# Kernel optimization log

Hardware: AMD Instinct MI355X
Metric: run time of the kernel (lower is better)

## Reference

```python
import jax, jax.numpy as jnp
import numpy as np

NUM_LAYERS = 3

def setup_inputs() -> dict:
    key = jax.random.key(0)
    k1, k2, k3, k4 = jax.random.split(key, 4)
    N, D, E = 100000, 128, 3200000
    x = jax.random.normal(k1, (N, D), dtype=jnp.float32)
    edge_row = jax.random.randint(k2, (E,), 0, N, dtype=jnp.int64 if jax.config.jax_enable_x64 else jnp.int32)
    edge_col = jax.random.randint(k3, (E,), 0, N, dtype=jnp.int64 if jax.config.jax_enable_x64 else jnp.int32)
    # normalized-adjacency-like positive values
    edge_val = jax.random.uniform(k4, (E,), dtype=jnp.float32)
    return {"x": x, "edge_row": edge_row, "edge_col": edge_col, "edge_val": edge_val}

def _spmm(edge_row, edge_col, edge_val, emb, num_nodes):
    # out[r] += val * emb[c]  -- sparse adjacency @ emb
    msgs = edge_val[:, None] * emb[edge_col]          # [E, D] gather + scale
    return jax.ops.segment_sum(msgs, edge_row, num_segments=num_nodes)

def reference(x, edge_row, edge_col, edge_val):
    N = x.shape[0]
    emb = x
    acc = x  # running sum over layer embeddings (layer 0 included)
    for _ in range(NUM_LAYERS):
        emb = _spmm(edge_row, edge_col, edge_val, emb, N)
        acc = acc + emb
    # mean over (num_layers + 1) stacked embeddings, without materializing the stack
    return acc / jnp.float32(NUM_LAYERS + 1)
```

## Files before the change

### kernel.cpp

```cpp
#include <hip/hip_runtime.h>

#define DIMS 128
#define RPB 64
#define CAP 3072
#define NBK_MAX 1600
#define NBINS 1024

typedef _Float16 half_t;
typedef _Float16 half2_t __attribute__((ext_vector_type(2)));

static __device__ __forceinline__ unsigned halfbits(float v) {
    half_t h = (half_t)v;
    unsigned short us;
    __builtin_memcpy(&us, &h, 2);
    return (unsigned)us;
}
static __device__ __forceinline__ half2_t h2(int b) { return __builtin_bit_cast(half2_t, b); }
static __device__ __forceinline__ int ih(half2_t h) { return __builtin_bit_cast(int, h); }

__global__ void cvt_kernel(const float* __restrict__ src, half_t* __restrict__ dst, int n2) {
    int i = blockIdx.x * blockDim.x + threadIdx.x;
    if (i >= n2) return;
    float2 v = reinterpret_cast<const float2*>(src)[i];
    half2_t h;
    h.x = (half_t)v.x;
    h.y = (half_t)v.y;
    reinterpret_cast<half2_t*>(&dst[0])[i] = h;
}

__global__ __launch_bounds__(512) void binA_kernel(
    const int* __restrict__ row, const int* __restrict__ col,
    const float* __restrict__ val, int E, int nbk,
    int* __restrict__ fill, int2* __restrict__ staged) {
    __shared__ int cnt[NBK_MAX];
    __shared__ int base[NBK_MAX];
    const int t = threadIdx.x;
    const int tile0 = blockIdx.x * 8192;
    for (int j = t; j < nbk; j += 512) cnt[j] = 0;
    __syncthreads();
    for (int k = 0; k < 4; ++k) {
        int e = tile0 + (k * 512 + t) * 4;
        if (e + 3 < E) {
            int4 r4 = *reinterpret_cast<const int4*>(&row[e]);
            atomicAdd(&cnt[r4.x >> 6], 1);
            atomicAdd(&cnt[r4.y >> 6], 1);
            atomicAdd(&cnt[r4.z >> 6], 1);
            atomicAdd(&cnt[r4.w >> 6], 1);
        } else {
            for (int j = e; j < E; ++j) atomicAdd(&cnt[row[j] >> 6], 1);
        }
    }
    __syncthreads();
    for (int j = t; j < nbk; j += 512) {
        int c = cnt[j];
        base[j] = c ? atomicAdd(&fill[j], c) : 0;
        cnt[j] = 0;
    }
    __syncthreads();
    for (int k = 0; k < 4; ++k) {
        int e = tile0 + (k * 512 + t) * 4;
        int n = (e + 3 < E) ? 4 : max(0, E - e);
        if (n == 4) {
            int4 r4 = *reinterpret_cast<const int4*>(&row[e]);
            int4 c4 = *reinterpret_cast<const int4*>(&col[e]);
            float4 v4 = *reinterpret_cast<const float4*>(&val[e]);
            int rr[4] = {r4.x, r4.y, r4.z, r4.w};
            int cc[4] = {c4.x, c4.y, c4.z, c4.w};
            float vv[4] = {v4.x, v4.y, v4.z, v4.w};
#pragma unroll
            for (int j = 0; j < 4; ++j) {
                int b = rr[j] >> 6;
                int p = base[b] + atomicAdd(&cnt[b], 1);
                if (p < CAP) {
                    unsigned hb = halfbits(vv[j]);
                    int2 pk;
                    pk.x = (int)(((unsigned)(rr[j] & 63) << 26) | ((unsigned)cc[j] << 8));
                    pk.y = (int)((hb << 16) | hb);
                    staged[(size_t)b * CAP + p] = pk;
                }
            }
        } else {
            for (int j = e; j < e + n; ++j) {
                int r = row[j];
                int b = r >> 6;
                int p = base[b] + atomicAdd(&cnt[b], 1);
                if (p < CAP) {
                    unsigned hb = halfbits(val[j]);
                    int2 pk;
                    pk.x = (int)(((unsigned)(r & 63) << 26) | ((unsigned)col[j] << 8));
                    pk.y = (int)((hb << 16) | hb);
                    staged[(size_t)b * CAP + p] = pk;
                }
            }
        }
    }
}

__global__ __launch_bounds__(512) void sort_bucket(
    const int* __restrict__ fill, int2* __restrict__ staged,
    int* __restrict__ rowinfo, int N) {
    __shared__ int2 outb[CAP];
    __shared__ int cur[NBINS];
    __shared__ int wsum[8];
    const int b = blockIdx.x;
    const int t = threadIdx.x;
    const int w = t >> 6, lane = t & 63;
    const int cnt = min(fill[b], CAP);
    int2* gb = staged + (size_t)b * CAP;

    cur[2 * t] = 0;
    cur[2 * t + 1] = 0;
    __syncthreads();
    for (int i = t; i < cnt; i += 512) {
        unsigned k = (unsigned)gb[i].x;
        int key = (int)((k >> 26) << 4) | (int)((k >> 21) & 0xF);
        atomicAdd(&cur[key], 1);
    }
    __syncthreads();
    int h0 = cur[2 * t], h1 = cur[2 * t + 1];
    int s = h0 + h1;
    int v = s;
    for (int d = 1; d < 64; d <<= 1) {
        int u = __shfl_up(v, d, 64);
        if (lane >= d) v += u;
    }
    if (lane == 63) wsum[w] = v;
    __syncthreads();
    if (t < 8) {
        int ws = wsum[t];
        int vv = ws;
        for (int d = 1; d < 8; d <<= 1) {
            int u = __shfl_up(vv, d, 64);
            if (t >= d) vv += u;
        }
        wsum[t] = vv - ws;
    }
    __syncthreads();
    int excl = wsum[w] + (v - s);
    cur[2 * t] = excl;
    cur[2 * t + 1] = excl + h0;
    __syncthreads();
    if (t < RPB) {
        int start = cur[t * 16];
        int end = (t == RPB - 1) ? cnt : cur[t * 16 + 16];
        int r = b * RPB + t;
        if (r < N) rowinfo[r] = (start << 16) | end;
    }
    __syncthreads();
    for (int i = t; i < cnt; i += 512) {
        int2 pk = gb[i];
        unsigned k = (unsigned)pk.x;
        int key = (int)((k >> 26) << 4) | (int)((k >> 21) & 0xF);
        int p = atomicAdd(&cur[key], 1);
        outb[p] = pk;
    }
    __syncthreads();
    for (int i = t; i < cnt; i += 512) gb[i] = outb[i];
}

template <int MODE>
__global__ __launch_bounds__(256) void spmm_kernel(
    const half_t* __restrict__ emb_in, const int* __restrict__ rowinfo,
    const int2* __restrict__ staged, int N,
    half_t* __restrict__ emb_out, half_t* __restrict__ acc_h,
    float* __restrict__ out) {
    const int r = (blockIdx.x * blockDim.x + threadIdx.x) >> 6;
    const int lane = threadIdx.x & 63;
    if (r >= N) return;
    const int info = rowinfo[r];
    const int start = info >> 16;
    const int end = info & 0xFFFF;
    const int2* eb = staged + (size_t)(r >> 6) * CAP;
    const char* tbl = reinterpret_cast<const char*>(emb_in);
    const int g = lane >> 4;
    const unsigned q16 = (unsigned)(lane & 15) << 4;

    half2_t acc[4][4];
#pragma unroll
    for (int u = 0; u < 4; ++u)
#pragma unroll
        for (int s = 0; s < 4; ++s) acc[u][s] = (half2_t)0;

    for (int base = start; base < end; base += 64) {
        const int cnt = min(64, end - base);
        int2 myE = make_int2(0, 0);
        if (base + lane < end) myE = eb[base + lane];

        int k = 0;
        for (; k + 16 <= cnt; k += 16) {
            int ex[4], ey[4];
#pragma unroll
            for (int u = 0; u < 4; ++u) {
                ex[u] = __shfl(myE.x, k + 4 * u + g, 64);
                ey[u] = __shfl(myE.y, k + 4 * u + g, 64);
            }
            int4 tv[4];
#pragma unroll
            for (int u = 0; u < 4; ++u) {
                unsigned voff = ((unsigned)ex[u] & 0x03FFFF00u) + q16;
                tv[u] = *reinterpret_cast<const int4*>(tbl + voff);
            }
#pragma unroll
            for (int u = 0; u < 4; ++u) {
                half2_t vv = h2(ey[u]);
                acc[u][0] = h2(tv[u].x) * vv + acc[u][0];
                acc[u][1] = h2(tv[u].y) * vv + acc[u][1];
                acc[u][2] = h2(tv[u].z) * vv + acc[u][2];
                acc[u][3] = h2(tv[u].w) * vv + acc[u][3];
            }
        }
        if (k < cnt) {
            int ex[4], ey[4];
#pragma unroll
            for (int u = 0; u < 4; ++u) {
                const int idx = k + 4 * u + g;
                const int cl = min(idx, cnt - 1);
                ex[u] = __shfl(myE.x, cl, 64);
                int tmp = __shfl(myE.y, cl, 64);
                ey[u] = (idx < cnt) ? tmp : 0;
            }
            int4 tv[4];
#pragma unroll
            for (int u = 0; u < 4; ++u) {
                unsigned voff = ((unsigned)ex[u] & 0x03FFFF00u) + q16;
                tv[u] = *reinterpret_cast<const int4*>(tbl + voff);
            }
#pragma unroll
            for (int u = 0; u < 4; ++u) {
                half2_t vv = h2(ey[u]);
                acc[u][0] = h2(tv[u].x) * vv + acc[u][0];
                acc[u][1] = h2(tv[u].y) * vv + acc[u][1];
                acc[u][2] = h2(tv[u].z) * vv + acc[u][2];
                acc[u][3] = h2(tv[u].w) * vv + acc[u][3];
            }
        }
    }

    half2_t a0 = (acc[0][0] + acc[1][0]) + (acc[2][0] + acc[3][0]);
    half2_t a1 = (acc[0][1] + acc[1][1]) + (acc[2][1] + acc[3][1]);
    half2_t a2 = (acc[0][2] + acc[1][2]) + (acc[2][2] + acc[3][2]);
    half2_t a3 = (acc[0][3] + acc[1][3]) + (acc[2][3] + acc[3][3]);
#pragma unroll
    for (int off = 16; off < 64; off <<= 1) {
        a0 = a0 + h2(__shfl_xor(ih(a0), off, 64));
        a1 = a1 + h2(__shfl_xor(ih(a1), off, 64));
        a2 = a2 + h2(__shfl_xor(ih(a2), off, 64));
        a3 = a3 + h2(__shfl_xor(ih(a3), off, 64));
    }

    if (lane < 16) {
        const size_t o = (size_t)r * DIMS + ((size_t)lane << 3);
        if (MODE == 0 || MODE == 1) {
            *reinterpret_cast<int4*>(&emb_out[o]) = make_int4(ih(a0), ih(a1), ih(a2), ih(a3));
        }
        if (MODE == 0) {
            int4 xv = *reinterpret_cast<const int4*>(&emb_in[o]);
            *reinterpret_cast<int4*>(&acc_h[o]) = make_int4(
                ih(h2(xv.x) + a0), ih(h2(xv.y) + a1), ih(h2(xv.z) + a2), ih(h2(xv.w) + a3));
        } else if (MODE == 1) {
            int4 cv = *reinterpret_cast<const int4*>(&acc_h[o]);
            *reinterpret_cast<int4*>(&acc_h[o]) = make_int4(
                ih(h2(cv.x) + a0), ih(h2(cv.y) + a1), ih(h2(cv.z) + a2), ih(h2(cv.w) + a3));
        } else {
            int4 cv = *reinterpret_cast<const int4*>(&acc_h[o]);
            half2_t c0 = h2(cv.x), c1 = h2(cv.y), c2 = h2(cv.z), c3 = h2(cv.w);
            float4 f0 = make_float4(((float)c0.x + (float)a0.x) * 0.25f,
                                    ((float)c0.y + (float)a0.y) * 0.25f,
                                    ((float)c1.x + (float)a1.x) * 0.25f,
                                    ((float)c1.y + (float)a1.y) * 0.25f);
            float4 f1 = make_float4(((float)c2.x + (float)a2.x) * 0.25f,
                                    ((float)c2.y + (float)a2.y) * 0.25f,
                                    ((float)c3.x + (float)a3.x) * 0.25f,
                                    ((float)c3.y + (float)a3.y) * 0.25f);
            float4* po = reinterpret_cast<float4*>(&out[o]);
            po[0] = f0;
            po[1] = f1;
        }
    }
}


extern "C" void kernel_launch(void* const* d_in, const int* in_sizes, int n_in,
                              void* d_out, int out_size, void* d_ws, size_t ws_size,
                              hipStream_t stream) {
    const float* x = (const float*)d_in[0];
    const int* erow = (const int*)d_in[1];
    const int* ecol = (const int*)d_in[2];
    const float* eval = (const float*)d_in[3];
    const int N = in_sizes[0] / DIMS;
    const int E = in_sizes[1];
    float* out = (float*)d_out;
    const int nbk = (N + RPB - 1) / RPB;

    char* ws = (char*)d_ws;
    size_t off = 0;
    auto carve = [&](size_t bytes) {
        void* p = ws + off;
        off = (off + bytes + 255) & ~(size_t)255;
        return p;
    };
    half_t* xh = (half_t*)carve((size_t)N * DIMS * sizeof(half_t));
    half_t* embB1 = (half_t*)carve((size_t)N * DIMS * sizeof(half_t));
    half_t* acc_h = (half_t*)carve((size_t)N * DIMS * sizeof(half_t));
    int2* staged = (int2*)carve((size_t)nbk * CAP * sizeof(int2));
    int* fill = (int*)carve((size_t)nbk * sizeof(int));
    int* rowinfo = (int*)carve((size_t)N * sizeof(int));
    (void)ws_size;

    hipMemsetAsync(fill, 0, (size_t)nbk * sizeof(int), stream);
    const int n2 = N * DIMS / 2;
    cvt_kernel<<<(n2 + 255) / 256, 256, 0, stream>>>(x, xh, n2);
    binA_kernel<<<(E + 8191) / 8192, 512, 0, stream>>>(erow, ecol, eval, E, nbk, fill, staged);
    sort_bucket<<<nbk, 512, 0, stream>>>(fill, staged, rowinfo, N);

    const int spmm_blocks = (N + 3) / 4;
    spmm_kernel<0><<<spmm_blocks, 256, 0, stream>>>(xh, rowinfo, staged, N, embB1, acc_h, out);
    spmm_kernel<1><<<spmm_blocks, 256, 0, stream>>>(embB1, rowinfo, staged, N, xh, acc_h, out);
    spmm_kernel<2><<<spmm_blocks, 256, 0, stream>>>(xh, rowinfo, staged, N, embB1, acc_h, out);
}
```

Before: 539.4 us.

## Process 16 rows per wave in column bands using per-bin offsets

Each wave now handles 16 rows: four 16-lane groups each own four rows and accumulate them directly. Edges are walked band by band, using the column bins already sorted in sort_bucket, so all active waves gather from the same slice of the embedding table. The per-row info array is replaced by a per-bucket table of 16-bit bin offsets, and the cross-group shuffle reduction is removed. In exchange, the loops now diverge across lane groups with one gather in flight per iteration, and a launch-bounds occupancy hint is added.

```diff
diff --git a/kernel.cpp b/kernel.cpp
--- a/kernel.cpp
+++ b/kernel.cpp
@@ -5,9 +5,12 @@
 #define CAP 3072
 #define NBK_MAX 1600
 #define NBINS 1024
+#define NBANDS 13
+#define RPW 16
 
 typedef _Float16 half_t;
 typedef _Float16 half2_t __attribute__((ext_vector_type(2)));
+typedef unsigned short ushort_t;
 
 static __device__ __forceinline__ unsigned halfbits(float v) {
     half_t h = (half_t)v;
@@ -98,7 +101,7 @@
 
 __global__ __launch_bounds__(512) void sort_bucket(
     const int* __restrict__ fill, int2* __restrict__ staged,
-    int* __restrict__ rowinfo, int N) {
+    ushort_t* __restrict__ binoff) {
     __shared__ int2 outb[CAP];
     __shared__ int cur[NBINS];
     __shared__ int wsum[8];
@@ -139,12 +142,11 @@
     int excl = wsum[w] + (v - s);
     cur[2 * t] = excl;
     cur[2 * t + 1] = excl + h0;
-    __syncthreads();
-    if (t < RPB) {
-        int start = cur[t * 16];
-        int end = (t == RPB - 1) ? cnt : cur[t * 16 + 16];
-        int r = b * RPB + t;
-        if (r < N) rowinfo[r] = (start << 16) | end;
+    {
+        ushort2 u2;
+        u2.x = (ushort_t)excl;
+        u2.y = (ushort_t)(excl + h0);
+        reinterpret_cast<ushort2*>(binoff + (size_t)b * NBINS)[t] = u2;
     }
     __syncthreads();
     for (int i = t; i < cnt; i += 512) {
@@ -159,21 +161,23 @@
 }
 
 template <int MODE>
-__global__ __launch_bounds__(256) void spmm_kernel(
-    const half_t* __restrict__ emb_in, const int* __restrict__ rowinfo,
+__global__ __launch_bounds__(256, 7) void spmm_kernel(
+    const half_t* __restrict__ emb_in, const ushort_t* __restrict__ binoff,
     const int2* __restrict__ staged, int N,
     half_t* __restrict__ emb_out, half_t* __restrict__ acc_h,
     float* __restrict__ out) {
-    const int r = (blockIdx.x * blockDim.x + threadIdx.x) >> 6;
+    const int wid = (blockIdx.x * blockDim.x + threadIdx.x) >> 6;
     const int lane = threadIdx.x & 63;
-    if (r >= N) return;
-    const int info = rowinfo[r];
-    const int start = info >> 16;
-    const int end = info & 0xFFFF;
-    const int2* eb = staged + (size_t)(r >> 6) * CAP;
+    const int r0 = wid * RPW;
+    if (r0 >= N) return;
+    const int bucket = r0 >> 6;
+    const int g = lane >> 4;
+    const int l16 = lane & 15;
+    const int gbase = g << 4;
+    const unsigned q16 = (unsigned)l16 << 4;
+    const int2* eb = staged + (size_t)bucket * CAP;
     const char* tbl = reinterpret_cast<const char*>(emb_in);
-    const int g = lane >> 4;
-    const unsigned q16 = (unsigned)(lane & 15) << 4;
+    const ushort_t* bo = binoff + (size_t)bucket * NBINS + (((r0 & 63) + (g << 2)) << 4);
 
     half2_t acc[4][4];
 #pragma unroll
@@ -181,75 +185,42 @@
 #pragma unroll
         for (int s = 0; s < 4; ++s) acc[u][s] = (half2_t)0;
 
-    for (int base = start; base < end; base += 64) {
-        const int cnt = min(64, end - base);
-        int2 myE = make_int2(0, 0);
-        if (base + lane < end) myE = eb[base + lane];
-
-        int k = 0;
-        for (; k + 16 <= cnt; k += 16) {
-            int ex[4], ey[4];
-#pragma unroll
-            for (int u = 0; u < 4; ++u) {
-                ex[u] = __shfl(myE.x, k + 4 * u + g, 64);
-                ey[u] = __shfl(myE.y, k + 4 * u + g, 64);
-            }
-            int4 tv[4];
-#pragma unroll
-            for (int u = 0; u < 4; ++u) {
-                unsigned voff = ((unsigned)ex[u] & 0x03FFFF00u) + q16;
-                tv[u] = *reinterpret_cast<const int4*>(tbl + voff);
-            }
-#pragma unroll
-            for (int u = 0; u < 4; ++u) {
-                half2_t vv = h2(ey[u]);
-                acc[u][0] = h2(tv[u].x) * vv + acc[u][0];
-                acc[u][1] = h2(tv[u].y) * vv + acc[u][1];
-                acc[u][2] = h2(tv[u].z) * vv + acc[u][2];
-                acc[u][3] = h2(tv[u].w) * vv + acc[u][3];
-            }
-        }
-        if (k < cnt) {
-            int ex[4], ey[4];
-#pragma unroll
-            for (int u = 0; u < 4; ++u) {
-                const int idx = k + 4 * u + g;
-                const int cl = min(idx, cnt - 1);
-                ex[u] = __shfl(myE.x, cl, 64);
-                int tmp = __shfl(myE.y, cl, 64);
-                ey[u] = (idx < cnt) ? tmp : 0;
-            }
-            int4 tv[4];
-#pragma unroll
-            for (int u = 0; u < 4; ++u) {
-                unsigned voff = ((unsigned)ex[u] & 0x03FFFF00u) + q16;
-                tv[u] = *reinterpret_cast<const int4*>(tbl + voff);
-            }
-#pragma unroll
-            for (int u = 0; u < 4; ++u) {
-                half2_t vv = h2(ey[u]);
-                acc[u][0] = h2(tv[u].x) * vv + acc[u][0];
-                acc[u][1] = h2(tv[u].y) * vv + acc[u][1];
-                acc[u][2] = h2(tv[u].z) * vv + acc[u][2];
-                acc[u][3] = h2(tv[u].w) * vv + acc[u][3];
-            }
-        }
-    }
-
-    half2_t a0 = (acc[0][0] + acc[1][0]) + (acc[2][0] + acc[3][0]);
-    half2_t a1 = (acc[0][1] + acc[1][1]) + (acc[2][1] + acc[3][1]);
-    half2_t a2 = (acc[0][2] + acc[1][2]) + (acc[2][2] + acc[3][2]);
-    half2_t a3 = (acc[0][3] + acc[1][3]) + (acc[2][3] + acc[3][3]);
-#pragma unroll
-    for (int off = 16; off < 64; off <<= 1) {
-        a0 = a0 + h2(__shfl_xor(ih(a0), off, 64));
-        a1 = a1 + h2(__shfl_xor(ih(a1), off, 64));
-        a2 = a2 + h2(__shfl_xor(ih(a2), off, 64));
-        a3 = a3 + h2(__shfl_xor(ih(a3), off, 64));
-    }
-
-    if (lane < 16) {
-        const size_t o = (size_t)r * DIMS + ((size_t)lane << 3);
+    int bs0 = (int)bo[0], bs1 = (int)bo[16], bs2 = (int)bo[32], bs3 = (int)bo[48];
+
+    for (int b = 0; b < NBANDS; ++b) {
+#define ROW_BAND(RR, BSV)                                                     \
+        {                                                                     \
+            const int be = (int)bo[RR * 16 + b + 1];                          \
+            for (int j0 = BSV; j0 < be; j0 += 16) {                           \
+                const int2 myE = eb[min(j0 + l16, be - 1)];                   \
+                const int cnt = min(16, be - j0);                             \
+                for (int j = 0; j < cnt; ++j) {                               \
+                    const int ex = __shfl(myE.x, gbase + j, 64);              \
+                    const int ey = __shfl(myE.y, gbase + j, 64);              \
+                    const unsigned voff = ((unsigned)ex & 0x03FFFF00u) + q16; \
+                    const int4 t4 = *reinterpret_cast<const int4*>(tbl + voff); \
+                    const half2_t vv = h2(ey);                                \
+                    acc[RR][0] = h2(t4.x) * vv + acc[RR][0];                  \
+                    acc[RR][1] = h2(t4.y) * vv + acc[RR][1];                  \
+                    acc[RR][2] = h2(t4.z) * vv + acc[RR][2];                  \
+                    acc[RR][3] = h2(t4.w) * vv + acc[RR][3];                  \
+                }                                                             \
+            }                                                                 \
+            BSV = be;                                                         \
+        }
+        ROW_BAND(0, bs0)
+        ROW_BAND(1, bs1)
+        ROW_BAND(2, bs2)
+        ROW_BAND(3, bs3)
+#undef ROW_BAND
+    }
+
+#pragma unroll
+    for (int rr = 0; rr < 4; ++rr) {
+        const int r = r0 + (g << 2) + rr;
+        const size_t o = (size_t)r * DIMS + ((size_t)l16 << 3);
+        const half2_t a0 = acc[rr][0], a1 = acc[rr][1];
+        const half2_t a2 = acc[rr][2], a3 = acc[rr][3];
         if (MODE == 0 || MODE == 1) {
             *reinterpret_cast<int4*>(&emb_out[o]) = make_int4(ih(a0), ih(a1), ih(a2), ih(a3));
         }
@@ -304,17 +275,18 @@
     half_t* acc_h = (half_t*)carve((size_t)N * DIMS * sizeof(half_t));
     int2* staged = (int2*)carve((size_t)nbk * CAP * sizeof(int2));
     int* fill = (int*)carve((size_t)nbk * sizeof(int));
-    int* rowinfo = (int*)carve((size_t)N * sizeof(int));
+    ushort_t* binoff = (ushort_t*)carve((size_t)nbk * NBINS * sizeof(ushort_t));
     (void)ws_size;
 
     hipMemsetAsync(fill, 0, (size_t)nbk * sizeof(int), stream);
     const int n2 = N * DIMS / 2;
     cvt_kernel<<<(n2 + 255) / 256, 256, 0, stream>>>(x, xh, n2);
     binA_kernel<<<(E + 8191) / 8192, 512, 0, stream>>>(erow, ecol, eval, E, nbk, fill, staged);
-    sort_bucket<<<nbk, 512, 0, stream>>>(fill, staged, rowinfo, N);
-
-    const int spmm_blocks = (N + 3) / 4;
-    spmm_kernel<0><<<spmm_blocks, 256, 0, stream>>>(xh, rowinfo, staged, N, embB1, acc_h, out);
-    spmm_kernel<1><<<spmm_blocks, 256, 0, stream>>>(embB1, rowinfo, staged, N, xh, acc_h, out);
-    spmm_kernel<2><<<spmm_blocks, 256, 0, stream>>>(xh, rowinfo, staged, N, embB1, acc_h, out);
-}
+    sort_bucket<<<nbk, 512, 0, stream>>>(fill, staged, binoff);
+
+    const int waves = (N + RPW - 1) / RPW;
+    const int spmm_blocks = (waves + 3) / 4;
+    spmm_kernel<0><<<spmm_blocks, 256, 0, stream>>>(xh, binoff, staged, N, embB1, acc_h, out);
+    spmm_kernel<1><<<spmm_blocks, 256, 0, stream>>>(embB1, binoff, staged, N, xh, acc_h, out);
+    spmm_kernel<2><<<spmm_blocks, 256, 0, stream>>>(xh, binoff, staged, N, embB1, acc_h, out);
+}
```

Result: slower. 588.0 us (+9.0%).
